# Performance work log

Measured on AMD Instinct MI355X. Metric: run time of the kernel, lower is better.

Reference implementation:

```python
import jax, jax.numpy as jnp
import numpy as np


def setup_inputs() -> dict:
    key = jax.random.key(0)
    ks = jax.random.split(key, 7)
    B, C, S, O = 4, 256, 4096, 256
    return {
        "X": jax.random.normal(ks[0], (B, C, S), dtype=jnp.float32),
        "Wq": jax.random.normal(ks[1], (O, C), dtype=jnp.float32) * 0.05,
        "bq": jax.random.normal(ks[2], (O,), dtype=jnp.float32) * 0.05,
        "Wk": jax.random.normal(ks[3], (O, C), dtype=jnp.float32) * 0.05,
        "bk": jax.random.normal(ks[4], (O,), dtype=jnp.float32) * 0.05,
        "Wv": jax.random.normal(ks[5], (O, C), dtype=jnp.float32) * 0.05,
        "bv": jax.random.normal(ks[6], (O,), dtype=jnp.float32) * 0.05,
        "n_heads": 4,
    }


def reference(X, Wq, bq, Wk, bk, Wv, bv, n_heads):
    # X: [B, C, S]; Conv1d kernel=1 == channel-mixing linear
    B, C, S = X.shape
    O = Wq.shape[0]
    H = n_heads
    W = O // H  # head dim

    def proj(Wm, bm):
        y = jnp.einsum('oc,bcs->bos', Wm, X) + bm[None, :, None]
        return y.reshape(B, H, W, S)

    q = proj(Wq, bq)  # [B,H,W,S]
    k = proj(Wk, bk)
    v = proj(Wv, bv)

    # scores = q^T @ k / sqrt(W): [B,H,S,S]
    scores = jnp.einsum('bhws,bhwt->bhst', q, k) / jnp.sqrt(jnp.asarray(W, X.dtype))
    # nonstandard: softmax over dim=-2 (the first S axis)
    scores = jax.nn.softmax(scores, axis=-2)
    # dropout is identity in eval mode
    # h = v @ scores: [B,H,W,S] @ [B,H,S,S] -> [B,H,W,S]
    h = jnp.einsum('bhws,bhst->bhwt', v, scores)
    return h.reshape(B, O, S)
```

## Files before the change

kernel.cpp:

```cpp
#include <hip/hip_runtime.h>
#include <stdint.h>


#define S_LEN 4096
#define HD 64
#define LOG2E 1.44269504088896f

typedef __attribute__((ext_vector_type(8))) __bf16 bf16x8;
typedef __attribute__((ext_vector_type(8))) unsigned short u16x8;
typedef __attribute__((ext_vector_type(4))) float f32x4;
typedef __attribute__((ext_vector_type(16))) float f32x16;
typedef __attribute__((ext_vector_type(4))) unsigned int u32x4;

__device__ __forceinline__ unsigned short f2bf(float f) {
    unsigned int u = __float_as_uint(f);
    u = (u + 0x7FFFu + ((u >> 16) & 1u)) >> 16;
    return (unsigned short)u;
}

__device__ __forceinline__ unsigned int cvt_pk_bf16(float lo, float hi) {
    unsigned int r;
    asm("v_cvt_pk_bf16_f32 %0, %1, %2" : "=v"(r) : "v"(lo), "v"(hi));
    return r;
}

#define PLSWAP(a, b) asm volatile("v_permlane32_swap_b32 %0, %1" : "+v"(a), "+v"(b))

__device__ __forceinline__ void gl16(const void* g, void* l) {
    __builtin_amdgcn_global_load_lds(
        (const __attribute__((address_space(1))) unsigned int*)g,
        (__attribute__((address_space(3))) unsigned int*)l, 16, 0, 0);
}

__global__ __launch_bounds__(256) void cvtX(const float* __restrict__ X,
                                            unsigned short* __restrict__ Xh) {
    __shared__ float LT[64][65];
    int tid = threadIdx.x;
    int id = blockIdx.x;
    int ct = id & 3;
    int st = (id >> 2) & 63;
    int b  = id >> 8;
    int sseg = (tid & 15) * 4;
    int crow = tid >> 4;
    const float* Xp = X + ((size_t)b << 20) + st * 64 + sseg;
#pragma unroll
    for (int p = 0; p < 4; p++) {
        int c = crow + p * 16;
        float4 v = *(const float4*)(Xp + ((size_t)(ct * 64 + c) << 12));
        LT[sseg + 0][c] = v.x;
        LT[sseg + 1][c] = v.y;
        LT[sseg + 2][c] = v.z;
        LT[sseg + 3][c] = v.w;
    }
    __syncthreads();
    int s = tid >> 2, cseg = (tid & 3) * 16;
    size_t ob = ((size_t)(b * S_LEN + st * 64 + s)) * 256 + ct * 64 + cseg;
#pragma unroll
    for (int hh = 0; hh < 2; hh++) {
        u16x8 vh;
#pragma unroll
        for (int i = 0; i < 8; i++) vh[i] = f2bf(LT[s][cseg + hh * 8 + i]);
        *(u16x8*)(Xh + ob + hh * 8) = vh;
    }
}

__global__ __launch_bounds__(256) void cvtW(const float* __restrict__ Wq,
                                            const float* __restrict__ Wk,
                                            const float* __restrict__ Wv,
                                            unsigned short* __restrict__ Wb) {
    int id = blockIdx.x;
    int z = id >> 5, blk = id & 31;
    const float* src = (z == 0) ? Wq : ((z == 1) ? Wk : Wv);
    int base = blk * 2048 + threadIdx.x * 8;
    u16x8 vh;
#pragma unroll
    for (int i = 0; i < 8; i++) vh[i] = f2bf(src[base + i]);
    *(u16x8*)(Wb + (size_t)z * 65536 + base) = vh;
}

__global__ __launch_bounds__(256) void proj_gemm(
    const unsigned short* __restrict__ Xh,
    const unsigned short* __restrict__ Wb,
    const float* __restrict__ bq, const float* __restrict__ bk, const float* __restrict__ bv,
    unsigned short* __restrict__ Qt, unsigned short* __restrict__ Kt,
    unsigned short* __restrict__ Vn) {
    int tid = threadIdx.x, lane = tid & 63, wv = tid >> 6;
    int l16 = lane & 15, lg = lane >> 4;
    int bid = blockIdx.x;
    int z = bid / 512;
    int r = bid % 512;
    int mBlk = r & 127, oBlk = r >> 7;

    const float* bias = (z == 0) ? bq : ((z == 1) ? bk : bv);
    const unsigned short* Wh = Wb + (size_t)z * 65536;

    int sBase = mBlk * 128 + (wv & 1) * 64;
    int oBase = oBlk * 64 + (wv >> 1) * 32;

    f32x4 acc[4][2] = {};

    const unsigned short* Ah_p = Xh + (size_t)(sBase + l16) * 256 + lg * 8;
    const unsigned short* Bh_p = Wh + (size_t)(oBase + l16) * 256 + lg * 8;

    for (int kk = 0; kk < 8; kk++) {
        int ko = kk * 32;
        bf16x8 ah[4], bh[2];
#pragma unroll
        for (int mt = 0; mt < 4; mt++)
            ah[mt] = *(const bf16x8*)(Ah_p + mt * 16 * 256 + ko);
#pragma unroll
        for (int nt = 0; nt < 2; nt++)
            bh[nt] = *(const bf16x8*)(Bh_p + nt * 16 * 256 + ko);
#pragma unroll
        for (int mt = 0; mt < 4; mt++)
#pragma unroll
            for (int nt = 0; nt < 2; nt++)
                acc[mt][nt] = __builtin_amdgcn_mfma_f32_16x16x32_bf16(ah[mt], bh[nt], acc[mt][nt], 0, 0, 0);
    }

    float b0 = bias[oBase + l16];
    float b1 = bias[oBase + 16 + l16];
    int b = mBlk >> 5;

    if (z < 2) {
        unsigned short* dst = (z == 0) ? Qt : Kt;
        float sc = (z == 1) ? (0.125f * LOG2E) : 1.0f;
        int head = oBlk;
        int d0 = (wv >> 1) * 32 + l16;
        size_t rowbase = ((size_t)(b * 4 + head)) * S_LEN;
#pragma unroll
        for (int mt = 0; mt < 4; mt++)
#pragma unroll
            for (int j = 0; j < 4; j++) {
                int s = (mBlk & 31) * 128 + (wv & 1) * 64 + mt * 16 + lg * 4 + j;
                size_t off = (rowbase + s) * HD;
                dst[off + d0]      = f2bf((acc[mt][0][j] + b0) * sc);
                dst[off + d0 + 16] = f2bf((acc[mt][1][j] + b1) * sc);
            }
    } else {
        __shared__ unsigned short TL[64][136];
        int o0l = (wv >> 1) * 32 + l16;
#pragma unroll
        for (int mt = 0; mt < 4; mt++) {
            int sl = (wv & 1) * 64 + mt * 16 + lg * 4;
            *(unsigned int*)&TL[o0l][sl]          = cvt_pk_bf16(acc[mt][0][0] + b0, acc[mt][0][1] + b0);
            *(unsigned int*)&TL[o0l][sl + 2]      = cvt_pk_bf16(acc[mt][0][2] + b0, acc[mt][0][3] + b0);
            *(unsigned int*)&TL[o0l + 16][sl]     = cvt_pk_bf16(acc[mt][1][0] + b1, acc[mt][1][1] + b1);
            *(unsigned int*)&TL[o0l + 16][sl + 2] = cvt_pk_bf16(acc[mt][1][2] + b1, acc[mt][1][3] + b1);
        }
        __syncthreads();
        int ol = tid >> 2, sc0 = (tid & 3) * 32;
        int bhIdx = b * 4 + oBlk;
        int sbase = (mBlk & 31) * 128 + sc0;
        size_t obase = (size_t)bhIdx * 262144 + (size_t)ol * 64;
#pragma unroll
        for (int u = 0; u < 4; u++) {
            int s = sbase + u * 8;
            size_t addr = obase + (size_t)(s >> 6) * 4096 + (s & 63);
            u16x8 v = *(u16x8*)&TL[ol][sc0 + u * 8];
            *(u16x8*)(Vn + addr) = v;
        }
    }
}

__global__ __launch_bounds__(512, 4) void attn_v10(const unsigned short* __restrict__ Qt,
                                                   const unsigned short* __restrict__ Kt,
                                                   const unsigned short* __restrict__ Vt2,
                                                   float* __restrict__ out) {
    __shared__ __align__(16) char smem[65536];
    int tid = threadIdx.x, lane = tid & 63, wv = tid >> 6;
    int l31 = lane & 31, h = lane >> 5;
    int g = wv >> 2, ws = wv & 3;

    int blk = blockIdx.x;
    int swz = (blk & 7) * 64 + (blk >> 3);
    int tblk = swz & 31, bh = swz >> 5;
    int t0 = tblk * 128 + ws * 32;

    const unsigned short* kp = Kt + ((size_t)bh * S_LEN + t0 + l31) * HD + h * 8;
    bf16x8 kf[4];
#pragma unroll
    for (int u = 0; u < 4; u++) kf[u] = *(const bf16x8*)(kp + u * 16);

    const char* Qg = (const char*)(Qt + (size_t)bh * S_LEN * HD);
    const char* Vg = (const char*)(Vt2 + (size_t)bh * 262144);

    int pos0 = ws * 2048 + lane * 16;
    int pos1 = pos0 + 1024;
    int r0 = pos0 >> 7, c0 = (pos0 >> 4) & 7;
    int r1 = pos1 >> 7, c1 = (pos1 >> 4) & 7;
    int src0 = r0 * 128 + ((c0 ^ (r0 & 7)) << 4);
    int src1 = r1 * 128 + ((c1 ^ (r1 & 7)) << 4);

    char* Qbase = smem + g * 16384;
    char* Vbase = smem + 32768 + g * 16384;

    const int rx = l31 & 7;
    int ch[4];
#pragma unroll
    for (int u = 0; u < 4; u++) ch[u] = (((u * 2 + h) ^ rx) << 4);
    const int rowb = l31 * 128;

    f32x16 oacc0 = {}, oacc1 = {}, lsumv = {};
    const f32x16 ZV = {};

#define STAGE10(p, t) do {                                  \
        const char* qg_ = Qg + (size_t)(t) * 8192;          \
        const char* vg_ = Vg + (size_t)(t) * 8192;          \
        gl16(qg_ + src0, Qbase + (p) * 8192 + ws * 2048);         \
        gl16(qg_ + src1, Qbase + (p) * 8192 + ws * 2048 + 1024);  \
        gl16(vg_ + src0, Vbase + (p) * 8192 + ws * 2048);         \
        gl16(vg_ + src1, Vbase + (p) * 8192 + ws * 2048 + 1024);  \
    } while (0)

    STAGE10(0, g);
    __syncthreads();

    for (int it = 0; it < 32; ++it) {
        char* Qb = Qbase + (it & 1) * 8192;
        char* Vb = Vbase + (it & 1) * 8192;
        if (it < 31) STAGE10((it & 1) ^ 1, 2 * it + 2 + g);

        __builtin_amdgcn_s_setprio(1);
        f32x16 s0, s1;
        {
            bf16x8 q = *(const bf16x8*)(Qb + rowb + ch[0]);
            s0 = __builtin_amdgcn_mfma_f32_32x32x16_bf16(q, kf[0], ZV, 0, 0, 0);
        }
#pragma unroll
        for (int u = 1; u < 4; u++) {
            bf16x8 q = *(const bf16x8*)(Qb + rowb + ch[u]);
            s0 = __builtin_amdgcn_mfma_f32_32x32x16_bf16(q, kf[u], s0, 0, 0, 0);
        }
        {
            bf16x8 q = *(const bf16x8*)(Qb + 4096 + rowb + ch[0]);
            s1 = __builtin_amdgcn_mfma_f32_32x32x16_bf16(q, kf[0], ZV, 0, 0, 0);
        }
#pragma unroll
        for (int u = 1; u < 4; u++) {
            bf16x8 q = *(const bf16x8*)(Qb + 4096 + rowb + ch[u]);
            s1 = __builtin_amdgcn_mfma_f32_32x32x16_bf16(q, kf[u], s1, 0, 0, 0);
        }
        __builtin_amdgcn_s_setprio(0);

#pragma unroll
        for (int r = 0; r < 16; r++) {
            s0[r] = __builtin_amdgcn_exp2f(s0[r]);
            s1[r] = __builtin_amdgcn_exp2f(s1[r]);
        }

        lsumv += s0;
        lsumv += s1;

        unsigned int W0[4][2], W1[4][2];
#pragma unroll
        for (int q = 0; q < 4; q++)
#pragma unroll
            for (int ip = 0; ip < 2; ip++) {
                W0[q][ip] = cvt_pk_bf16(s0[4 * q + 2 * ip], s0[4 * q + 2 * ip + 1]);
                W1[q][ip] = cvt_pk_bf16(s1[4 * q + 2 * ip], s1[4 * q + 2 * ip + 1]);
            }
        u32x4 pw0, pw1, pw2, pw3;
        {
            unsigned int a0 = W0[0][0], b0 = W0[1][0]; PLSWAP(a0, b0);
            unsigned int a1 = W0[0][1], b1 = W0[1][1]; PLSWAP(a1, b1);
            pw0 = (u32x4){a0, a1, b0, b1};
            unsigned int c0s = W0[2][0], d0s = W0[3][0]; PLSWAP(c0s, d0s);
            unsigned int c1s = W0[2][1], d1s = W0[3][1]; PLSWAP(c1s, d1s);
            pw1 = (u32x4){c0s, c1s, d0s, d1s};
            unsigned int e0 = W1[0][0], f0 = W1[1][0]; PLSWAP(e0, f0);
            unsigned int e1 = W1[0][1], f1 = W1[1][1]; PLSWAP(e1, f1);
            pw2 = (u32x4){e0, e1, f0, f1};
            unsigned int g0 = W1[2][0], h0 = W1[3][0]; PLSWAP(g0, h0);
            unsigned int g1 = W1[2][1], h1 = W1[3][1]; PLSWAP(g1, h1);
            pw3 = (u32x4){g0, g1, h0, h1};
        }
        bf16x8 pb0 = *(bf16x8*)&pw0, pb1 = *(bf16x8*)&pw1;
        bf16x8 pb2 = *(bf16x8*)&pw2, pb3 = *(bf16x8*)&pw3;

        __builtin_amdgcn_s_setprio(1);
#pragma unroll
        for (int b2 = 0; b2 < 4; b2++) {
            bf16x8 pb = (b2 == 0) ? pb0 : (b2 == 1) ? pb1 : (b2 == 2) ? pb2 : pb3;
            bf16x8 v0 = *(const bf16x8*)(Vb + rowb + ch[b2]);
            bf16x8 v1 = *(const bf16x8*)(Vb + 4096 + rowb + ch[b2]);
            oacc0 = __builtin_amdgcn_mfma_f32_32x32x16_bf16(v0, pb, oacc0, 0, 0, 0);
            oacc1 = __builtin_amdgcn_mfma_f32_32x32x16_bf16(v1, pb, oacc1, 0, 0, 0);
        }
        __builtin_amdgcn_s_setprio(0);

        __syncthreads();
    }

    float l_lane = 0.f;
#pragma unroll
    for (int r = 0; r < 16; r++) l_lane += lsumv[r];
    float l = l_lane + __shfl_xor(l_lane, 32);

    if (g == 1) {
        float* ml = (float*)(smem + ws * 256);
        ml[lane] = l;
        float* ob = (float*)(smem + 32768 + ws * 8192) + lane * 32;
#pragma unroll
        for (int r = 0; r < 16; r++) {
            ob[(((r >> 2) ^ rx) << 2) + (r & 3)]       = oacc0[r];
            ob[((((r >> 2) + 4) ^ rx) << 2) + (r & 3)] = oacc1[r];
        }
    }
    __syncthreads();
    if (g == 0) {
        const float* ml = (const float*)(smem + ws * 256);
        float lB = ml[lane];
        const float* ob = (const float*)(smem + 32768 + ws * 8192) + lane * 32;
        float rinv = 1.0f / (l + lB);

        float* op = out + (size_t)(bh * 64) * S_LEN + t0 + l31;
#pragma unroll
        for (int r = 0; r < 16; r++) {
            int d = (r & 3) + 8 * (r >> 2) + 4 * h;
            float vB0 = ob[(((r >> 2) ^ rx) << 2) + (r & 3)];
            float vB1 = ob[((((r >> 2) + 4) ^ rx) << 2) + (r & 3)];
            op[(size_t)d * S_LEN]        = (oacc0[r] + vB0) * rinv;
            op[(size_t)(d + 32) * S_LEN] = (oacc1[r] + vB1) * rinv;
        }
    }
}

extern "C" void kernel_launch(void* const* d_in, const int* in_sizes, int n_in,
                              void* d_out, int out_size, void* d_ws, size_t ws_size,
                              hipStream_t stream) {
    const float* X  = (const float*)d_in[0];
    const float* Wq = (const float*)d_in[1];
    const float* bq = (const float*)d_in[2];
    const float* Wk = (const float*)d_in[3];
    const float* bk = (const float*)d_in[4];
    const float* Wv = (const float*)d_in[5];
    const float* bv = (const float*)d_in[6];
    float* out = (float*)d_out;

    const size_t ELEMS = (size_t)16 * S_LEN * HD;
    unsigned short* Qt = (unsigned short*)d_ws;
    unsigned short* Kt = Qt + ELEMS;
    unsigned short* Vn = Kt + ELEMS;
    unsigned short* Wb = Vn + ELEMS;

    unsigned short* Xh = (unsigned short*)d_out;

    cvtX<<<1024, 256, 0, stream>>>(X, Xh);
    cvtW<<<96, 256, 0, stream>>>(Wq, Wk, Wv, Wb);
    proj_gemm<<<1536, 256, 0, stream>>>(Xh, Wb, bq, bk, bv, Qt, Kt, Vn);
    attn_v10<<<512, 512, 0, stream>>>(Qt, Kt, Vn, out);
}
```

Baseline: 132.1 us.

## Merge QKV projections per block, compute softmax sums via MFMA, drop LDS swizzle

After: 118.5 us. 1.11x faster.

```diff
diff --git a/kernel.cpp b/kernel.cpp
--- a/kernel.cpp
+++ b/kernel.cpp
@@ -84,86 +84,85 @@
     const float* __restrict__ bq, const float* __restrict__ bk, const float* __restrict__ bv,
     unsigned short* __restrict__ Qt, unsigned short* __restrict__ Kt,
     unsigned short* __restrict__ Vn) {
+    __shared__ unsigned short TL[64][136];
     int tid = threadIdx.x, lane = tid & 63, wv = tid >> 6;
     int l16 = lane & 15, lg = lane >> 4;
     int bid = blockIdx.x;
-    int z = bid / 512;
-    int r = bid % 512;
-    int mBlk = r & 127, oBlk = r >> 7;
-
-    const float* bias = (z == 0) ? bq : ((z == 1) ? bk : bv);
-    const unsigned short* Wh = Wb + (size_t)z * 65536;
+    int mBlk = bid & 127, oBlk = bid >> 7;
 
     int sBase = mBlk * 128 + (wv & 1) * 64;
     int oBase = oBlk * 64 + (wv >> 1) * 32;
-
-    f32x4 acc[4][2] = {};
+    int b = mBlk >> 5;
 
     const unsigned short* Ah_p = Xh + (size_t)(sBase + l16) * 256 + lg * 8;
-    const unsigned short* Bh_p = Wh + (size_t)(oBase + l16) * 256 + lg * 8;
-
-    for (int kk = 0; kk < 8; kk++) {
-        int ko = kk * 32;
-        bf16x8 ah[4], bh[2];
-#pragma unroll
-        for (int mt = 0; mt < 4; mt++)
-            ah[mt] = *(const bf16x8*)(Ah_p + mt * 16 * 256 + ko);
-#pragma unroll
-        for (int nt = 0; nt < 2; nt++)
-            bh[nt] = *(const bf16x8*)(Bh_p + nt * 16 * 256 + ko);
-#pragma unroll
-        for (int mt = 0; mt < 4; mt++)
+    const float* biases[3] = {bq, bk, bv};
+
+    for (int z = 0; z < 3; z++) {
+        const float* bias = biases[z];
+        const unsigned short* Bh_p = Wb + (size_t)z * 65536 + (size_t)(oBase + l16) * 256 + lg * 8;
+
+        f32x4 acc[4][2] = {};
+        for (int kk = 0; kk < 8; kk++) {
+            int ko = kk * 32;
+            bf16x8 ah[4], bh[2];
+#pragma unroll
+            for (int mt = 0; mt < 4; mt++)
+                ah[mt] = *(const bf16x8*)(Ah_p + mt * 16 * 256 + ko);
 #pragma unroll
             for (int nt = 0; nt < 2; nt++)
-                acc[mt][nt] = __builtin_amdgcn_mfma_f32_16x16x32_bf16(ah[mt], bh[nt], acc[mt][nt], 0, 0, 0);
-    }
-
-    float b0 = bias[oBase + l16];
-    float b1 = bias[oBase + 16 + l16];
-    int b = mBlk >> 5;
-
-    if (z < 2) {
-        unsigned short* dst = (z == 0) ? Qt : Kt;
-        float sc = (z == 1) ? (0.125f * LOG2E) : 1.0f;
-        int head = oBlk;
-        int d0 = (wv >> 1) * 32 + l16;
-        size_t rowbase = ((size_t)(b * 4 + head)) * S_LEN;
-#pragma unroll
-        for (int mt = 0; mt < 4; mt++)
-#pragma unroll
-            for (int j = 0; j < 4; j++) {
-                int s = (mBlk & 31) * 128 + (wv & 1) * 64 + mt * 16 + lg * 4 + j;
-                size_t off = (rowbase + s) * HD;
-                dst[off + d0]      = f2bf((acc[mt][0][j] + b0) * sc);
-                dst[off + d0 + 16] = f2bf((acc[mt][1][j] + b1) * sc);
+                bh[nt] = *(const bf16x8*)(Bh_p + nt * 16 * 256 + ko);
+#pragma unroll
+            for (int mt = 0; mt < 4; mt++)
+#pragma unroll
+                for (int nt = 0; nt < 2; nt++)
+                    acc[mt][nt] = __builtin_amdgcn_mfma_f32_16x16x32_bf16(ah[mt], bh[nt], acc[mt][nt], 0, 0, 0);
+        }
+
+        float b0 = bias[oBase + l16];
+        float b1 = bias[oBase + 16 + l16];
+
+        if (z < 2) {
+            unsigned short* dst = (z == 0) ? Qt : Kt;
+            float sc = (z == 1) ? (0.125f * LOG2E) : 1.0f;
+            int head = oBlk;
+            int d0 = (wv >> 1) * 32 + l16;
+            size_t rowbase = ((size_t)(b * 4 + head)) * S_LEN;
+#pragma unroll
+            for (int mt = 0; mt < 4; mt++)
+#pragma unroll
+                for (int j = 0; j < 4; j++) {
+                    int s = (mBlk & 31) * 128 + (wv & 1) * 64 + mt * 16 + lg * 4 + j;
+                    size_t off = (rowbase + s) * HD;
+                    dst[off + d0]      = f2bf((acc[mt][0][j] + b0) * sc);
+                    dst[off + d0 + 16] = f2bf((acc[mt][1][j] + b1) * sc);
+                }
+        } else {
+            int o0l = (wv >> 1) * 32 + l16;
+#pragma unroll
+            for (int mt = 0; mt < 4; mt++) {
+                int sl = (wv & 1) * 64 + mt * 16 + lg * 4;
+                *(unsigned int*)&TL[o0l][sl]          = cvt_pk_bf16(acc[mt][0][0] + b0, acc[mt][0][1] + b0);
+                *(unsigned int*)&TL[o0l][sl + 2]      = cvt_pk_bf16(acc[mt][0][2] + b0, acc[mt][0][3] + b0);
+                *(unsigned int*)&TL[o0l + 16][sl]     = cvt_pk_bf16(acc[mt][1][0] + b1, acc[mt][1][1] + b1);
+                *(unsigned int*)&TL[o0l + 16][sl + 2] = cvt_pk_bf16(acc[mt][1][2] + b1, acc[mt][1][3] + b1);
             }
-    } else {
-        __shared__ unsigned short TL[64][136];
-        int o0l = (wv >> 1) * 32 + l16;
-#pragma unroll
-        for (int mt = 0; mt < 4; mt++) {
-            int sl = (wv & 1) * 64 + mt * 16 + lg * 4;
-            *(unsigned int*)&TL[o0l][sl]          = cvt_pk_bf16(acc[mt][0][0] + b0, acc[mt][0][1] + b0);
-            *(unsigned int*)&TL[o0l][sl + 2]      = cvt_pk_bf16(acc[mt][0][2] + b0, acc[mt][0][3] + b0);
-            *(unsigned int*)&TL[o0l + 16][sl]     = cvt_pk_bf16(acc[mt][1][0] + b1, acc[mt][1][1] + b1);
-            *(unsigned int*)&TL[o0l + 16][sl + 2] = cvt_pk_bf16(acc[mt][1][2] + b1, acc[mt][1][3] + b1);
-        }
-        __syncthreads();
-        int ol = tid >> 2, sc0 = (tid & 3) * 32;
-        int bhIdx = b * 4 + oBlk;
-        int sbase = (mBlk & 31) * 128 + sc0;
-        size_t obase = (size_t)bhIdx * 262144 + (size_t)ol * 64;
-#pragma unroll
-        for (int u = 0; u < 4; u++) {
-            int s = sbase + u * 8;
-            size_t addr = obase + (size_t)(s >> 6) * 4096 + (s & 63);
-            u16x8 v = *(u16x8*)&TL[ol][sc0 + u * 8];
-            *(u16x8*)(Vn + addr) = v;
-        }
-    }
-}
-
-__global__ __launch_bounds__(512, 4) void attn_v10(const unsigned short* __restrict__ Qt,
+            __syncthreads();
+            int ol = tid >> 2, sc0 = (tid & 3) * 32;
+            int bhIdx = b * 4 + oBlk;
+            int sbase = (mBlk & 31) * 128 + sc0;
+            size_t obase = (size_t)bhIdx * 262144 + (size_t)ol * 64;
+#pragma unroll
+            for (int u = 0; u < 4; u++) {
+                int s = sbase + u * 8;
+                size_t addr = obase + (size_t)(s >> 6) * 4096 + (s & 63);
+                u16x8 v = *(u16x8*)&TL[ol][sc0 + u * 8];
+                *(u16x8*)(Vn + addr) = v;
+            }
+        }
+    }
+}
+
+__global__ __launch_bounds__(512, 4) void attn_v11(const unsigned short* __restrict__ Qt,
                                                    const unsigned short* __restrict__ Kt,
                                                    const unsigned short* __restrict__ Vt2,
                                                    float* __restrict__ out) {
@@ -185,60 +184,61 @@
     const char* Qg = (const char*)(Qt + (size_t)bh * S_LEN * HD);
     const char* Vg = (const char*)(Vt2 + (size_t)bh * 262144);
 
-    int pos0 = ws * 2048 + lane * 16;
-    int pos1 = pos0 + 1024;
-    int r0 = pos0 >> 7, c0 = (pos0 >> 4) & 7;
-    int r1 = pos1 >> 7, c1 = (pos1 >> 4) & 7;
-    int src0 = r0 * 128 + ((c0 ^ (r0 & 7)) << 4);
-    int src1 = r1 * 128 + ((c1 ^ (r1 & 7)) << 4);
+    int srcA = lane * 128 + ws * 32;
+    int srcB = srcA + 16;
 
     char* Qbase = smem + g * 16384;
     char* Vbase = smem + 32768 + g * 16384;
 
+    int ch[4];
+#pragma unroll
+    for (int u = 0; u < 4; u++) ch[u] = ((u * 2 + h) << 10);
+    const int rowb = l31 * 16;
     const int rx = l31 & 7;
-    int ch[4];
-#pragma unroll
-    for (int u = 0; u < 4; u++) ch[u] = (((u * 2 + h) ^ rx) << 4);
-    const int rowb = l31 * 128;
-
-    f32x16 oacc0 = {}, oacc1 = {}, lsumv = {};
+
+    f32x16 oacc0 = {}, oacc1 = {}, lacc = {};
     const f32x16 ZV = {};
 
-#define STAGE10(p, t) do {                                  \
+    u16x8 ou;
+#pragma unroll
+    for (int i = 0; i < 8; i++) ou[i] = 0x3F80;
+    bf16x8 ones = (bf16x8)ou;
+
+#define STAGE11(p, t) do {                                  \
         const char* qg_ = Qg + (size_t)(t) * 8192;          \
         const char* vg_ = Vg + (size_t)(t) * 8192;          \
-        gl16(qg_ + src0, Qbase + (p) * 8192 + ws * 2048);         \
-        gl16(qg_ + src1, Qbase + (p) * 8192 + ws * 2048 + 1024);  \
-        gl16(vg_ + src0, Vbase + (p) * 8192 + ws * 2048);         \
-        gl16(vg_ + src1, Vbase + (p) * 8192 + ws * 2048 + 1024);  \
+        gl16(qg_ + srcA, Qbase + (p) * 8192 + ws * 2048);         \
+        gl16(qg_ + srcB, Qbase + (p) * 8192 + ws * 2048 + 1024);  \
+        gl16(vg_ + srcA, Vbase + (p) * 8192 + ws * 2048);         \
+        gl16(vg_ + srcB, Vbase + (p) * 8192 + ws * 2048 + 1024);  \
     } while (0)
 
-    STAGE10(0, g);
+    STAGE11(0, g);
     __syncthreads();
 
     for (int it = 0; it < 32; ++it) {
         char* Qb = Qbase + (it & 1) * 8192;
         char* Vb = Vbase + (it & 1) * 8192;
-        if (it < 31) STAGE10((it & 1) ^ 1, 2 * it + 2 + g);
+        if (it < 31) STAGE11((it & 1) ^ 1, 2 * it + 2 + g);
 
         __builtin_amdgcn_s_setprio(1);
         f32x16 s0, s1;
         {
-            bf16x8 q = *(const bf16x8*)(Qb + rowb + ch[0]);
+            bf16x8 q = *(const bf16x8*)(Qb + ch[0] + rowb);
             s0 = __builtin_amdgcn_mfma_f32_32x32x16_bf16(q, kf[0], ZV, 0, 0, 0);
         }
 #pragma unroll
         for (int u = 1; u < 4; u++) {
-            bf16x8 q = *(const bf16x8*)(Qb + rowb + ch[u]);
+            bf16x8 q = *(const bf16x8*)(Qb + ch[u] + rowb);
             s0 = __builtin_amdgcn_mfma_f32_32x32x16_bf16(q, kf[u], s0, 0, 0, 0);
         }
         {
-            bf16x8 q = *(const bf16x8*)(Qb + 4096 + rowb + ch[0]);
+            bf16x8 q = *(const bf16x8*)(Qb + ch[0] + rowb + 512);
             s1 = __builtin_amdgcn_mfma_f32_32x32x16_bf16(q, kf[0], ZV, 0, 0, 0);
         }
 #pragma unroll
         for (int u = 1; u < 4; u++) {
-            bf16x8 q = *(const bf16x8*)(Qb + 4096 + rowb + ch[u]);
+            bf16x8 q = *(const bf16x8*)(Qb + ch[u] + rowb + 512);
             s1 = __builtin_amdgcn_mfma_f32_32x32x16_bf16(q, kf[u], s1, 0, 0, 0);
         }
         __builtin_amdgcn_s_setprio(0);
@@ -248,9 +248,6 @@
             s0[r] = __builtin_amdgcn_exp2f(s0[r]);
             s1[r] = __builtin_amdgcn_exp2f(s1[r]);
         }
-
-        lsumv += s0;
-        lsumv += s1;
 
         unsigned int W0[4][2], W1[4][2];
 #pragma unroll
@@ -282,21 +279,18 @@
 #pragma unroll
         for (int b2 = 0; b2 < 4; b2++) {
             bf16x8 pb = (b2 == 0) ? pb0 : (b2 == 1) ? pb1 : (b2 == 2) ? pb2 : pb3;
-            bf16x8 v0 = *(const bf16x8*)(Vb + rowb + ch[b2]);
-            bf16x8 v1 = *(const bf16x8*)(Vb + 4096 + rowb + ch[b2]);
+            bf16x8 v0 = *(const bf16x8*)(Vb + ch[b2] + rowb);
+            bf16x8 v1 = *(const bf16x8*)(Vb + ch[b2] + rowb + 512);
             oacc0 = __builtin_amdgcn_mfma_f32_32x32x16_bf16(v0, pb, oacc0, 0, 0, 0);
             oacc1 = __builtin_amdgcn_mfma_f32_32x32x16_bf16(v1, pb, oacc1, 0, 0, 0);
+            lacc  = __builtin_amdgcn_mfma_f32_32x32x16_bf16(ones, pb, lacc, 0, 0, 0);
         }
         __builtin_amdgcn_s_setprio(0);
 
         __syncthreads();
     }
 
-    float l_lane = 0.f;
-#pragma unroll
-    for (int r = 0; r < 16; r++) l_lane += lsumv[r];
-    float l = l_lane + __shfl_xor(l_lane, 32);
-
+    float l = lacc[0];
     if (g == 1) {
         float* ml = (float*)(smem + ws * 256);
         ml[lane] = l;
@@ -348,6 +342,6 @@
 
     cvtX<<<1024, 256, 0, stream>>>(X, Xh);
     cvtW<<<96, 256, 0, stream>>>(Wq, Wk, Wv, Wb);
-    proj_gemm<<<1536, 256, 0, stream>>>(Xh, Wb, bq, bk, bv, Qt, Kt, Vn);
-    attn_v10<<<512, 512, 0, stream>>>(Qt, Kt, Vn, out);
-}
+    proj_gemm<<<512, 256, 0, stream>>>(Xh, Wb, bq, bk, bv, Qt, Kt, Vn);
+    attn_v11<<<512, 512, 0, stream>>>(Qt, Kt, Vn, out);
+}
```
